# Kernel tuning notes

Hardware: AMD Instinct MI355X
Metric: run time of the kernel (lower is better)

## Reference

```python
import jax, jax.numpy as jnp
import numpy as np

B, V, I, O, G = 128, 1024, 512, 512, 16


def setup_inputs() -> dict:
    key = jax.random.key(0)
    kx, kg, kw, kb = jax.random.split(key, 4)
    x = jax.random.normal(kx, (B, V, I), dtype=jnp.float32)
    group_index = jax.random.randint(kg, (V,), 0, G, dtype=jnp.int64)
    weight = jax.random.normal(kw, (G, O, I), dtype=jnp.float32) * (1.0 / np.sqrt(I))
    bias = jax.random.normal(kb, (G, O), dtype=jnp.float32) * 0.01
    return {"x": x, "group_index": group_index, "weight": weight, "bias": bias}


def reference(x, group_index, weight, bias):
    # Gather per-node weights/bias (torch.index_select along group dim)
    w = weight[group_index]          # [V, O, I]
    b = bias[group_index]            # [V, O]
    # einsum '...VI,VOI->...VO' with leading batch dim b
    out = jnp.einsum('bvi,voi->bvo', x, w)  # [B, V, O]
    return out + b
```

## Files before the change

kernel.cpp:

```cpp
#include <hip/hip_runtime.h>
#include <stdint.h>

#define B_DIM 128
#define V_DIM 1024
#define I_DIM 512
#define O_DIM 512
#define G_DIM 16

#define TM 128
#define TN 512
#define BK 32
#define KSTEPS (I_DIM / BK)
#define TILE_ELEMS (O_DIM * BK)

typedef __bf16 bf16x8 __attribute__((ext_vector_type(8)));
typedef __bf16 bf16x4 __attribute__((ext_vector_type(4)));
typedef float  f32x4  __attribute__((ext_vector_type(4)));

#define GLOBAL_AS __attribute__((address_space(1)))
#define LDS_AS    __attribute__((address_space(3)))

__device__ __forceinline__ void dma16(const void* g, void* l) {
    __builtin_amdgcn_global_load_lds((const GLOBAL_AS uint32_t*)g,
                                     (LDS_AS uint32_t*)l, 16, 0, 0);
}

__device__ __forceinline__ bf16x8 cvt8(f32x4 lo, f32x4 hi) {
    bf16x8 r;
    r[0] = (__bf16)lo[0]; r[1] = (__bf16)lo[1]; r[2] = (__bf16)lo[2]; r[3] = (__bf16)lo[3];
    r[4] = (__bf16)hi[0]; r[5] = (__bf16)hi[1]; r[6] = (__bf16)hi[2]; r[7] = (__bf16)hi[3];
    return r;
}

__global__ __launch_bounds__(256) void convert_w_packed(const float* __restrict__ src,
                                                        __bf16* __restrict__ dst) {
    const int cid  = blockIdx.x * 256 + threadIdx.x;
    const int c    = cid & 63;
    const int olin = cid >> 6;
    const int o    = olin & (O_DIM - 1);
    const int g    = olin >> 9;
    const int kt   = c >> 2;
    const int cc   = c & 3;
    const int s    = cc ^ ((o >> 1) & 3);
    const float4* sp = (const float4*)(src + (size_t)olin * I_DIM + c * 8);
    float4 v0 = sp[0], v1 = sp[1];
    bf16x8 r;
    r[0] = (__bf16)v0.x; r[1] = (__bf16)v0.y; r[2] = (__bf16)v0.z; r[3] = (__bf16)v0.w;
    r[4] = (__bf16)v1.x; r[5] = (__bf16)v1.y; r[6] = (__bf16)v1.z; r[7] = (__bf16)v1.w;
    *(bf16x8*)&dst[((size_t)(g * KSTEPS + kt) * O_DIM + o) * BK + s * 8] = r;
}

__global__ __launch_bounds__(512, 2)
void glinear_mfma(const float* __restrict__ x,
                  const int*   __restrict__ gidx,
                  const __bf16* __restrict__ wb,
                  const float* __restrict__ bias,
                  float*       __restrict__ out) {
    const int v = blockIdx.x;
    const int g = gidx[v];

    __shared__ float  lds_a[TM * BK];
    __shared__ __bf16 lds_b[TN * BK];

    const int tid  = threadIdx.x;
    const int lane = tid & 63;
    const int wave = tid >> 6;
    const int wm   = (wave & 1) * 64;
    const int wn   = (wave >> 1) * 128;
    const int fr   = lane & 15;
    const int c0   = lane >> 4;

    const int ar  = lane >> 3;
    const int agc = (lane & 7) ^ ar;
    const float* aga[2];
#pragma unroll
    for (int j = 0; j < 2; ++j) {
        const int r = wave * 16 + j * 8 + ar;
        aga[j] = x + ((size_t)r * V_DIM + v) * I_DIM + agc * 4;
    }
    const __bf16* btile = wb + (size_t)g * KSTEPS * TILE_ELEMS;

    f32x4 acc[4][8];
    const f32x4 zero = {0.f, 0.f, 0.f, 0.f};
#pragma unroll
    for (int ms = 0; ms < 4; ++ms)
#pragma unroll
        for (int ns = 0; ns < 8; ++ns) acc[ms][ns] = zero;

#pragma unroll
    for (int j = 0; j < 2; ++j)
        dma16(aga[j], &lds_a[(wave * 16 + j * 8) * BK]);
#pragma unroll
    for (int j = 0; j < 4; ++j)
        dma16(btile + (wave * 64 + j * 16) * BK + lane * 8,
              &lds_b[(wave * 64 + j * 16) * BK]);
    __syncthreads();

    const int ar7 = fr & 7;
    const int as0 = (2 * c0)     ^ ar7;
    const int as1 = (2 * c0 + 1) ^ ar7;
    const int bs  = c0 ^ ((fr >> 1) & 3);

    for (int kt = 0; kt < KSTEPS; ++kt) {
        bf16x8 av[4], bv[8];
#pragma unroll
        for (int t = 0; t < 4; ++t) {
            const float* ab = &lds_a[(wm + t * 16 + fr) * BK];
            f32x4 alo = *(const f32x4*)(ab + as0 * 4);
            f32x4 ahi = *(const f32x4*)(ab + as1 * 4);
            av[t] = cvt8(alo, ahi);
        }
#pragma unroll
        for (int t = 0; t < 8; ++t)
            bv[t] = *(const bf16x8*)&lds_b[(wn + t * 16 + fr) * BK + bs * 8];
        __syncthreads();

        if (kt < KSTEPS - 1) {
#pragma unroll
            for (int j = 0; j < 2; ++j)
                dma16(aga[j] + (kt + 1) * BK, &lds_a[(wave * 16 + j * 8) * BK]);
            const __bf16* bt = btile + (size_t)(kt + 1) * TILE_ELEMS;
#pragma unroll
            for (int j = 0; j < 4; ++j)
                dma16(bt + (wave * 64 + j * 16) * BK + lane * 8,
                      &lds_b[(wave * 64 + j * 16) * BK]);
        }

#pragma unroll
        for (int ms = 0; ms < 4; ++ms)
#pragma unroll
            for (int ns = 0; ns < 8; ++ns)
                acc[ms][ns] = __builtin_amdgcn_mfma_f32_16x16x32_bf16(
                    av[ms], bv[ns], acc[ms][ns], 0, 0, 0);

        if (kt < KSTEPS - 1)
            __syncthreads();
    }

    const float* bptr = bias + (size_t)g * O_DIM;
    float bvals[8];
#pragma unroll
    for (int ns = 0; ns < 8; ++ns) bvals[ns] = bptr[wn + ns * 16 + fr];

    const int rbase = (lane >> 4) * 4;
#pragma unroll
    for (int ms = 0; ms < 4; ++ms) {
#pragma unroll
        for (int r = 0; r < 4; ++r) {
            const int m = wm + ms * 16 + rbase + r;
            float* orow = out + ((size_t)m * V_DIM + v) * O_DIM;
#pragma unroll
            for (int ns = 0; ns < 8; ++ns)
                orow[wn + ns * 16 + fr] = acc[ms][ns][r] + bvals[ns];
        }
    }
}

#define FBTN 128
#define LDK 40
__device__ __forceinline__ __bf16 f2bf(float f) {
    unsigned u = __builtin_bit_cast(unsigned, f);
    u += 0x7fffu + ((u >> 16) & 1u);
    unsigned short h = (unsigned short)(u >> 16);
    return __builtin_bit_cast(__bf16, h);
}
__device__ __forceinline__ void cvt_store16(__bf16* dst, const float4* src) {
    bf16x8 lo, hi;
    lo[0] = f2bf(src[0].x); lo[1] = f2bf(src[0].y); lo[2] = f2bf(src[0].z); lo[3] = f2bf(src[0].w);
    lo[4] = f2bf(src[1].x); lo[5] = f2bf(src[1].y); lo[6] = f2bf(src[1].z); lo[7] = f2bf(src[1].w);
    hi[0] = f2bf(src[2].x); hi[1] = f2bf(src[2].y); hi[2] = f2bf(src[2].z); hi[3] = f2bf(src[2].w);
    hi[4] = f2bf(src[3].x); hi[5] = f2bf(src[3].y); hi[6] = f2bf(src[3].z); hi[7] = f2bf(src[3].w);
    *(bf16x8*)dst = lo; *(bf16x8*)(dst + 8) = hi;
}
__global__ __launch_bounds__(256, 2)
void glinear_fb(const float* __restrict__ x, const int* __restrict__ gidx,
                const float* __restrict__ w, const float* __restrict__ bias,
                float* __restrict__ out) {
    const int v = blockIdx.y, n0 = blockIdx.x * FBTN, g = gidx[v];
    __shared__ __bf16 lds_a[2][TM * LDK];
    __shared__ __bf16 lds_b[2][FBTN * LDK];
    const int tid = threadIdx.x, lane = tid & 63, wave = tid >> 6;
    const int wm = (wave & 1) * 64, wn = (wave >> 1) * 64;
    const int fr = lane & 15, kg = (lane >> 4) * 8;
    const int srow = tid >> 1, skh = (tid & 1) * 16;
    const float* xrow = x + ((size_t)srow * V_DIM + v) * I_DIM + skh;
    const float* wrow = w + (((size_t)g * O_DIM) + n0 + srow) * I_DIM + skh;
    const int soff = srow * LDK + skh;
    f32x4 acc[4][4];
    const f32x4 zero = {0.f, 0.f, 0.f, 0.f};
#pragma unroll
    for (int ms = 0; ms < 4; ++ms)
#pragma unroll
        for (int ns = 0; ns < 4; ++ns) acc[ms][ns] = zero;
    {
        float4 ax[4], bx[4];
#pragma unroll
        for (int i = 0; i < 4; ++i) { ax[i] = ((const float4*)xrow)[i]; bx[i] = ((const float4*)wrow)[i]; }
        cvt_store16(&lds_a[0][soff], ax); cvt_store16(&lds_b[0][soff], bx);
    }
    __syncthreads();
    for (int kt = 0; kt < KSTEPS; ++kt) {
        const int cur = kt & 1, nxt = cur ^ 1;
        float4 ax[4], bx[4];
        if (kt < KSTEPS - 1) {
            const float* xp = xrow + (kt + 1) * BK;
            const float* wp = wrow + (kt + 1) * BK;
#pragma unroll
            for (int i = 0; i < 4; ++i) { ax[i] = ((const float4*)xp)[i]; bx[i] = ((const float4*)wp)[i]; }
        }
        bf16x8 av[4], bv[4];
#pragma unroll
        for (int t = 0; t < 4; ++t) {
            av[t] = *(const bf16x8*)&lds_a[cur][(wm + t * 16 + fr) * LDK + kg];
            bv[t] = *(const bf16x8*)&lds_b[cur][(wn + t * 16 + fr) * LDK + kg];
        }
#pragma unroll
        for (int ms = 0; ms < 4; ++ms)
#pragma unroll
            for (int ns = 0; ns < 4; ++ns)
                acc[ms][ns] = __builtin_amdgcn_mfma_f32_16x16x32_bf16(av[ms], bv[ns], acc[ms][ns], 0, 0, 0);
        if (kt < KSTEPS - 1) { cvt_store16(&lds_a[nxt][soff], ax); cvt_store16(&lds_b[nxt][soff], bx); }
        __syncthreads();
    }
    const float* bptr = bias + (size_t)g * O_DIM + n0;
    float bvals[4];
#pragma unroll
    for (int ns = 0; ns < 4; ++ns) bvals[ns] = bptr[wn + ns * 16 + fr];
    const int rbase = (lane >> 4) * 4;
#pragma unroll
    for (int ms = 0; ms < 4; ++ms)
#pragma unroll
        for (int r = 0; r < 4; ++r) {
            const int m = wm + ms * 16 + rbase + r;
            float* orow = out + ((size_t)m * V_DIM + v) * O_DIM + n0;
#pragma unroll
            for (int ns = 0; ns < 4; ++ns) orow[wn + ns * 16 + fr] = acc[ms][ns][r] + bvals[ns];
        }
}

extern "C" void kernel_launch(void* const* d_in, const int* in_sizes, int n_in,
                              void* d_out, int out_size, void* d_ws, size_t ws_size,
                              hipStream_t stream) {
    const float* x    = (const float*)d_in[0];
    const int*   gidx = (const int*)d_in[1];
    const float* w    = (const float*)d_in[2];
    const float* bias = (const float*)d_in[3];
    float*       out  = (float*)d_out;

    const size_t w_elems = (size_t)G_DIM * O_DIM * I_DIM;
    const size_t need    = w_elems * sizeof(__bf16);

    if (ws_size >= need) {
        __bf16* wb = (__bf16*)d_ws;
        convert_w_packed<<<(int)(w_elems / 8 / 256), 256, 0, stream>>>(w, wb);
        glinear_mfma<<<dim3(V_DIM), 512, 0, stream>>>(x, gidx, wb, bias, out);
    } else {
        dim3 grid(O_DIM / FBTN, V_DIM);
        glinear_fb<<<grid, 256, 0, stream>>>(x, gidx, w, bias, out);
    }
}
```

Before: 536.0 us.

## Triple-buffer LDS tiles with prefetch distance two and explicit vmcnt waits

The single shared buffer, with two barriers per K-step, becomes a three-stage ring of A/B tiles. Each stage is prefetched two K-steps ahead and synchronised with `s_waitcnt vmcnt(6)` plus one `s_barrier` per step, and the last step is peeled out of the loop. The aim is to hide global-to-LDS load latency behind the MFMA work and cut the barrier count. The cost is that LDS use grows to about 144KB per block and launch bounds drop to one block per CU, which halves occupancy.

Result: no change. 537.8 us (+0.3%).

```diff
diff --git a/kernel.cpp b/kernel.cpp
--- a/kernel.cpp
+++ b/kernel.cpp
@@ -50,7 +50,18 @@
     *(bf16x8*)&dst[((size_t)(g * KSTEPS + kt) * O_DIM + o) * BK + s * 8] = r;
 }
 
-__global__ __launch_bounds__(512, 2)
+#define STAGE(kts, s) do {                                                    \
+    _Pragma("unroll")                                                         \
+    for (int j_ = 0; j_ < 2; ++j_)                                            \
+        dma16(aga[j_] + (kts) * BK, &lds_a[s][(wave * 16 + j_ * 8) * BK]);    \
+    const __bf16* bt_ = btile + (size_t)(kts) * TILE_ELEMS;                   \
+    _Pragma("unroll")                                                         \
+    for (int j_ = 0; j_ < 4; ++j_)                                            \
+        dma16(bt_ + (wave * 64 + j_ * 16) * BK + lane * 8,                    \
+              &lds_b[s][(wave * 64 + j_ * 16) * BK]);                         \
+} while (0)
+
+__global__ __launch_bounds__(512, 1)
 void glinear_mfma(const float* __restrict__ x,
                   const int*   __restrict__ gidx,
                   const __bf16* __restrict__ wb,
@@ -59,8 +70,8 @@
     const int v = blockIdx.x;
     const int g = gidx[v];
 
-    __shared__ float  lds_a[TM * BK];
-    __shared__ __bf16 lds_b[TN * BK];
+    __shared__ float  lds_a[3][TM * BK];
+    __shared__ __bf16 lds_b[3][TN * BK];
 
     const int tid  = threadIdx.x;
     const int lane = tid & 63;
@@ -87,44 +98,34 @@
 #pragma unroll
         for (int ns = 0; ns < 8; ++ns) acc[ms][ns] = zero;
 
-#pragma unroll
-    for (int j = 0; j < 2; ++j)
-        dma16(aga[j], &lds_a[(wave * 16 + j * 8) * BK]);
-#pragma unroll
-    for (int j = 0; j < 4; ++j)
-        dma16(btile + (wave * 64 + j * 16) * BK + lane * 8,
-              &lds_b[(wave * 64 + j * 16) * BK]);
-    __syncthreads();
+    STAGE(0, 0);
+    STAGE(1, 1);
 
     const int ar7 = fr & 7;
     const int as0 = (2 * c0)     ^ ar7;
     const int as1 = (2 * c0 + 1) ^ ar7;
     const int bs  = c0 ^ ((fr >> 1) & 3);
 
-    for (int kt = 0; kt < KSTEPS; ++kt) {
+    int cs = 0;
+    for (int kt = 0; kt < KSTEPS - 1; ++kt) {
+        asm volatile("s_waitcnt vmcnt(6)" ::: "memory");
+        asm volatile("s_barrier" ::: "memory");
+        if (kt + 2 < KSTEPS) {
+            int ns3 = cs + 2; if (ns3 >= 3) ns3 -= 3;
+            STAGE(kt + 2, ns3);
+        }
+
         bf16x8 av[4], bv[8];
 #pragma unroll
         for (int t = 0; t < 4; ++t) {
-            const float* ab = &lds_a[(wm + t * 16 + fr) * BK];
+            const float* ab = &lds_a[cs][(wm + t * 16 + fr) * BK];
             f32x4 alo = *(const f32x4*)(ab + as0 * 4);
             f32x4 ahi = *(const f32x4*)(ab + as1 * 4);
             av[t] = cvt8(alo, ahi);
         }
 #pragma unroll
         for (int t = 0; t < 8; ++t)
-            bv[t] = *(const bf16x8*)&lds_b[(wn + t * 16 + fr) * BK + bs * 8];
-        __syncthreads();
-
-        if (kt < KSTEPS - 1) {
-#pragma unroll
-            for (int j = 0; j < 2; ++j)
-                dma16(aga[j] + (kt + 1) * BK, &lds_a[(wave * 16 + j * 8) * BK]);
-            const __bf16* bt = btile + (size_t)(kt + 1) * TILE_ELEMS;
-#pragma unroll
-            for (int j = 0; j < 4; ++j)
-                dma16(bt + (wave * 64 + j * 16) * BK + lane * 8,
-                      &lds_b[(wave * 64 + j * 16) * BK]);
-        }
+            bv[t] = *(const bf16x8*)&lds_b[cs][(wn + t * 16 + fr) * BK + bs * 8];
 
 #pragma unroll
         for (int ms = 0; ms < 4; ++ms)
@@ -133,8 +134,29 @@
                 acc[ms][ns] = __builtin_amdgcn_mfma_f32_16x16x32_bf16(
                     av[ms], bv[ns], acc[ms][ns], 0, 0, 0);
 
-        if (kt < KSTEPS - 1)
-            __syncthreads();
+        if (++cs == 3) cs = 0;
+    }
+
+    {
+        asm volatile("s_waitcnt vmcnt(0)" ::: "memory");
+        asm volatile("s_barrier" ::: "memory");
+        bf16x8 av[4], bv[8];
+#pragma unroll
+        for (int t = 0; t < 4; ++t) {
+            const float* ab = &lds_a[cs][(wm + t * 16 + fr) * BK];
+            f32x4 alo = *(const f32x4*)(ab + as0 * 4);
+            f32x4 ahi = *(const f32x4*)(ab + as1 * 4);
+            av[t] = cvt8(alo, ahi);
+        }
+#pragma unroll
+        for (int t = 0; t < 8; ++t)
+            bv[t] = *(const bf16x8*)&lds_b[cs][(wn + t * 16 + fr) * BK + bs * 8];
+#pragma unroll
+        for (int ms = 0; ms < 4; ++ms)
+#pragma unroll
+            for (int ns = 0; ns < 8; ++ns)
+                acc[ms][ns] = __builtin_amdgcn_mfma_f32_16x16x32_bf16(
+                    av[ms], bv[ns], acc[ms][ns], 0, 0, 0);
     }
 
     const float* bptr = bias + (size_t)g * O_DIM;
```
